# Kernel tuning notes

Measured on AMD Instinct MI355X. Metric: run time of the kernel, lower is better.

Reference implementation:

```python
import jax, jax.numpy as jnp
import numpy as np

# dims: batch, d_features(m), n_subsets, sub_size(k=ceil(m/n)), heads, d_k, d_v, conv kernel, d_out
B, M, N, K, H, DK, DV, KER, D = 512, 4096, 64, 64, 8, 32, 4, 3, 4096
DOUT_PER = D // N  # d_out_per_subset = 64
EPS_LN = 1e-5      # torch nn.LayerNorm default eps


def setup_inputs() -> dict:
    key = jax.random.key(0)
    ks = jax.random.split(key, 8)
    s = 0.02  # xavier-like scale
    return {
        "features": jax.random.normal(ks[0], (B, M), dtype=jnp.float32),
        # per-head permutation of the m feature indices (f_shuffle(m, h, seeds))
        "shuffled_index": jnp.argsort(jax.random.uniform(ks[1], (H, M)), axis=1).astype(jnp.int32),
        "gamma": jnp.ones((M,), jnp.float32),
        "beta": jnp.zeros((M,), jnp.float32),
        "W_q": (jax.random.normal(ks[2], (H * DK, K)) * s).astype(jnp.float32),   # Linear(k, h*d_k)
        "W_k": (jax.random.normal(ks[3], (H, DK, K)) * s).astype(jnp.float32),    # grouped Conv1d(h, h*d_k, kernel=k, stride=k)
        "W_v1": (jax.random.normal(ks[4], (H, DV, KER)) * s).astype(jnp.float32), # grouped Conv1d(h, h*d_v, kernel)
        "W_v2": (jax.random.normal(ks[5], (H, DV)) * s).astype(jnp.float32),      # grouped Conv1d(h*d_v, h, 1)
        "W_fc": (jax.random.normal(ks[6], (DOUT_PER, H * K)) * s).astype(jnp.float32),
    }


def reference(features, shuffled_index, gamma, beta, W_q, W_k, W_v1, W_v2, W_fc):
    b = features.shape[0]
    # LayerNorm over m (query path only)
    mu = features.mean(-1, keepdims=True)
    var = ((features - mu) ** 2).mean(-1, keepdims=True)
    q_in = (features - mu) / jnp.sqrt(var + EPS_LN) * gamma + beta

    # shuffled gather: [b, H, M]  (k*n == m here so k_pad/q_pad are no-ops)
    sf = features[:, shuffled_index]

    # query: [b, n, k] -> Linear(k, h*d_k) -> [b, H, N, DK]
    q = jnp.einsum('bnk,ek->bne', q_in.reshape(b, N, K), W_q)
    q = q.reshape(b, N, H, DK).transpose(0, 2, 1, 3)

    # key: grouped conv kernel=stride=k == per-subset contraction -> [b, H, DK, N]
    kf = sf.reshape(b, H, N, K)
    key_ = jnp.einsum('bhnk,hdk->bhdn', kf, W_k)

    # value: [b, N, H, K], right-pad by KER-1, depthwise conv -> relu -> 1x1 conv -> +residual
    v = kf.transpose(0, 2, 1, 3)  # [b, N, H, K]
    vp = jnp.pad(v, ((0, 0), (0, 0), (0, 0), (0, KER - 1)))
    win = jnp.stack([vp[..., t:t + K] for t in range(KER)], axis=-1)  # [b,N,H,K,KER]
    v1 = jnp.einsum('bnhpt,hdt->bnhdp', win, W_v1)
    v2 = jnp.einsum('bnhdp,hd->bnhp', jax.nn.relu(v1), W_v2)
    v = (v2 + v).transpose(0, 2, 1, 3)  # [b, H, N, K]

    # scaled dot-product attention, temperature = sqrt(m)
    attn = jax.nn.softmax(jnp.einsum('bhqd,bhdk->bhqk', q, key_) / jnp.sqrt(jnp.float32(M)), axis=-1)
    out = jnp.einsum('bhqk,bhks->bhqs', attn, v)           # [b, H, N, K]
    out = out.transpose(0, 2, 1, 3).reshape(b, N, H * K)   # [b, N, H*K]
    out = jnp.einsum('bnf,of->bno', out, W_fc).reshape(b, N * DOUT_PER)
    return out, attn.reshape(b * H, N, N)
```

## Files before the change

kernel.cpp:

```cpp
#include <hip/hip_runtime.h>

typedef __bf16 v8bf __attribute__((ext_vector_type(8)));
typedef __bf16 v4bf __attribute__((ext_vector_type(4)));
typedef __bf16 v2bf __attribute__((ext_vector_type(2)));
typedef float  v4f  __attribute__((ext_vector_type(4)));
typedef float  v2f  __attribute__((ext_vector_type(2)));
typedef unsigned long long u64;

namespace {

constexpr int kB = 512, kM = 4096, kH = 8;


__global__ __launch_bounds__(256) void k0_weights(
    const float* __restrict__ Wq, const float* __restrict__ Wk,
    const float* __restrict__ Wfc,
    __bf16* __restrict__ wq, __bf16* __restrict__ wk, __bf16* __restrict__ wfc,
    float* __restrict__ out) {
  int i = blockIdx.x * 256 + threadIdx.x;
  float4 z = make_float4(0.f, 0.f, 0.f, 0.f);
#pragma unroll
  for (int j = 0; j < 4; ++j) reinterpret_cast<float4*>(out)[i + j * 131072] = z;
  if (i < 16384) {
    int e = i >> 6, k = i & 63;
    int dst = ((e >> 4) * 2 + (k >> 5)) * 512 + (e & 15) * 32 + (k & 31);
    wq[dst] = (__bf16)(Wq[i] * 0.015625f);
  } else if (i < 32768) {
    int j = i - 16384;
    int e = j >> 6, k = j & 63;
    int dst = ((e >> 4) * 2 + (k >> 5)) * 512 + (e & 15) * 32 + (k & 31);
    wk[dst] = (__bf16)Wk[j];
  } else if (i < 65536) {
    int j = i - 32768;
    int o = j >> 9, f = j & 511;
    int dst = ((o >> 4) * 16 + (f >> 5)) * 512 + (o & 15) * 32 + (f & 31);
    wfc[dst] = (__bf16)Wfc[j];
  }
}

__global__ __launch_bounds__(256, 4) void k_fused(
    const float* __restrict__ feat, const int* __restrict__ sidx,
    const float* __restrict__ gamma, const float* __restrict__ beta,
    const __bf16* __restrict__ wq, const __bf16* __restrict__ wk,
    const float* __restrict__ Wv1, const float* __restrict__ Wv2,
    const __bf16* __restrict__ wfc, float* __restrict__ out) {
  __shared__ __align__(16) __bf16 smem[19968];
  __shared__ float red[4];
  __bf16* s_feat = smem;
  __bf16* s_qin  = smem + 4096;
  __bf16* s_kf   = smem + 8192;
  __bf16* s_K    = smem + 12800;
  __bf16* s_vT   = smem + 15360;
  __bf16* s_sc   = s_kf;

  const int b = blockIdx.x, half = blockIdx.y, h0 = 4 * half;
  const int t = threadIdx.x, w = t >> 6, lane = t & 63;
  const int quad = lane >> 4, l16 = lane & 15;
  const int myrow = 16 * w + l16;

  const float4* frow4 = reinterpret_cast<const float4*>(feat + (size_t)b * kM);
  const float4* g4  = reinterpret_cast<const float4*>(gamma);
  const float4* be4 = reinterpret_cast<const float4*>(beta);
  float4 xs[4];
  float s = 0.f;
#pragma unroll
  for (int j = 0; j < 4; ++j) {
    xs[j] = frow4[t + j * 256];
    s += xs[j].x + xs[j].y + xs[j].z + xs[j].w;
  }
  int4 idxc[4], idxn[4];
  {
    const int* ibase = sidx + (size_t)h0 * kM + myrow * 64 + 8 * quad;
#pragma unroll
    for (int p = 0; p < 4; ++p)
      idxc[p] = *(const int4*)(ibase + 32 * (p >> 1) + 4 * (p & 1));
  }
#pragma unroll
  for (int o = 32; o > 0; o >>= 1) s += __shfl_xor(s, o);
  if (lane == 0) red[w] = s;
  __syncthreads();
  const float mu = (red[0] + red[1] + red[2] + red[3]) * (1.f / kM);
  float var_p = 0.f;
#pragma unroll
  for (int j = 0; j < 4; ++j) {
    float d0 = xs[j].x - mu, d1 = xs[j].y - mu, d2 = xs[j].z - mu, d3 = xs[j].w - mu;
    var_p += d0 * d0 + d1 * d1 + d2 * d2 + d3 * d3;
  }
#pragma unroll
  for (int o = 32; o > 0; o >>= 1) var_p += __shfl_xor(var_p, o);
  __syncthreads();
  if (lane == 0) red[w] = var_p;
  __syncthreads();
  const float var  = (red[0] + red[1] + red[2] + red[3]) * (1.f / kM);
  const float rstd = rsqrtf(var + 1e-5f);
#pragma unroll
  for (int j = 0; j < 4; ++j) {
    const int i4 = t + j * 256;
    float4 g = g4[i4], bt = be4[i4];
    v4bf fb, qb;
    fb[0] = (__bf16)xs[j].x; fb[1] = (__bf16)xs[j].y;
    fb[2] = (__bf16)xs[j].z; fb[3] = (__bf16)xs[j].w;
    qb[0] = (__bf16)((xs[j].x - mu) * rstd * g.x + bt.x);
    qb[1] = (__bf16)((xs[j].y - mu) * rstd * g.y + bt.y);
    qb[2] = (__bf16)((xs[j].z - mu) * rstd * g.z + bt.z);
    qb[3] = (__bf16)((xs[j].w - mu) * rstd * g.w + bt.w);
    *(v4bf*)(s_feat + 4 * i4) = fb;
    const int n = i4 >> 4, k = 4 * (t & 15);
    const int dst = ((n >> 4) * 2 + (k >> 5)) * 512 + (n & 15) * 32 + (k & 31);
    *(v4bf*)(s_qin + dst) = qb;
  }
  __syncthreads();

  v4f acc[4] = {{0.f, 0.f, 0.f, 0.f}, {0.f, 0.f, 0.f, 0.f},
                {0.f, 0.f, 0.f, 0.f}, {0.f, 0.f, 0.f, 0.f}};

  for (int it = 0; it < 4; ++it) {
    const int h = h0 + it;

    v8bf aq;
    {
      v4f dq0 = {0.f, 0.f, 0.f, 0.f}, dq1 = {0.f, 0.f, 0.f, 0.f};
#pragma unroll
      for (int kt = 0; kt < 2; ++kt) {
        v8bf a  = *(const v8bf*)(s_qin + (2 * w + kt) * 512 + l16 * 32 + 8 * quad);
        v8bf b0 = *(const v8bf*)(wq + (size_t)(4 * h + kt) * 512 + l16 * 32 + 8 * quad);
        v8bf b1 = *(const v8bf*)(wq + (size_t)(4 * h + 2 + kt) * 512 + l16 * 32 + 8 * quad);
        dq0 = __builtin_amdgcn_mfma_f32_16x16x32_bf16(b0, a, dq0, 0, 0, 0);
        dq1 = __builtin_amdgcn_mfma_f32_16x16x32_bf16(b1, a, dq1, 0, 0, 0);
      }
      v4bf p0, p1;
#pragma unroll
      for (int r = 0; r < 4; ++r) { p0[r] = (__bf16)dq0[r]; p1[r] = (__bf16)dq1[r]; }
      const u64 P0 = __builtin_bit_cast(u64, p0), P1 = __builtin_bit_cast(u64, p1);
      const int qs = 16 * (2 * (quad & 1));
      u64 s0p0 = __shfl(P0, l16 + qs),      s0p1 = __shfl(P1, l16 + qs);
      u64 s1p0 = __shfl(P0, l16 + qs + 16), s1p1 = __shfl(P1, l16 + qs + 16);
      v4bf lo = __builtin_bit_cast(v4bf, (quad >> 1) ? s0p1 : s0p0);
      v4bf hi = __builtin_bit_cast(v4bf, (quad >> 1) ? s1p1 : s1p0);
#pragma unroll
      for (int r = 0; r < 4; ++r) { aq[r] = lo[r]; aq[4 + r] = hi[r]; }
    }

    if (it < 3) {
      const int* ibase = sidx + (size_t)(h + 1) * kM + myrow * 64 + 8 * quad;
#pragma unroll
      for (int p = 0; p < 4; ++p)
        idxn[p] = *(const int4*)(ibase + 32 * (p >> 1) + 4 * (p & 1));
    }

    v8bf a0, a1;
    a0[0] = s_feat[idxc[0].x]; a0[1] = s_feat[idxc[0].y];
    a0[2] = s_feat[idxc[0].z]; a0[3] = s_feat[idxc[0].w];
    a0[4] = s_feat[idxc[1].x]; a0[5] = s_feat[idxc[1].y];
    a0[6] = s_feat[idxc[1].z]; a0[7] = s_feat[idxc[1].w];
    a1[0] = s_feat[idxc[2].x]; a1[1] = s_feat[idxc[2].y];
    a1[2] = s_feat[idxc[2].z]; a1[3] = s_feat[idxc[2].w];
    a1[4] = s_feat[idxc[3].x]; a1[5] = s_feat[idxc[3].y];
    a1[6] = s_feat[idxc[3].z]; a1[7] = s_feat[idxc[3].w];
    *(v8bf*)(s_kf + myrow * 72 + 8 * quad)      = a0;
    *(v8bf*)(s_kf + myrow * 72 + 32 + 8 * quad) = a1;
    if (t < 64) { v8bf z = {}; *(v8bf*)(s_kf + t * 72 + 64) = z; }

    {
      v4f dk0 = {0.f, 0.f, 0.f, 0.f}, dk1 = {0.f, 0.f, 0.f, 0.f};
      v8bf b00 = *(const v8bf*)(wk + (size_t)(4 * h + 0) * 512 + l16 * 32 + 8 * quad);
      v8bf b10 = *(const v8bf*)(wk + (size_t)(4 * h + 2) * 512 + l16 * 32 + 8 * quad);
      dk0 = __builtin_amdgcn_mfma_f32_16x16x32_bf16(b00, a0, dk0, 0, 0, 0);
      dk1 = __builtin_amdgcn_mfma_f32_16x16x32_bf16(b10, a0, dk1, 0, 0, 0);
      v8bf b01 = *(const v8bf*)(wk + (size_t)(4 * h + 1) * 512 + l16 * 32 + 8 * quad);
      v8bf b11 = *(const v8bf*)(wk + (size_t)(4 * h + 3) * 512 + l16 * 32 + 8 * quad);
      dk0 = __builtin_amdgcn_mfma_f32_16x16x32_bf16(b01, a1, dk0, 0, 0, 0);
      dk1 = __builtin_amdgcn_mfma_f32_16x16x32_bf16(b11, a1, dk1, 0, 0, 0);
      v4bf p0, p1;
#pragma unroll
      for (int r = 0; r < 4; ++r) { p0[r] = (__bf16)dk0[r]; p1[r] = (__bf16)dk1[r]; }
      *(v4bf*)(s_K + myrow * 40 + 4 * quad)      = p0;
      *(v4bf*)(s_K + myrow * 40 + 16 + 4 * quad) = p1;
    }
    __syncthreads();

    {
      const int n = lane, p0c = w * 16;
      float w1[4][3], w2[4];
#pragma unroll
      for (int d = 0; d < 4; ++d) {
#pragma unroll
        for (int c = 0; c < 3; ++c) w1[d][c] = Wv1[(h * 4 + d) * 3 + c];
        w2[d] = Wv2[h * 4 + d];
      }
      v8bf xa = *(const v8bf*)(s_kf + n * 72 + p0c);
      v8bf xb = *(const v8bf*)(s_kf + n * 72 + p0c + 8);
      v2bf xc = *(const v2bf*)(s_kf + n * 72 + p0c + 16);
      v2f x2[10];
#pragma unroll
      for (int j = 0; j < 8; ++j) { x2[j][0] = (float)xa[j]; x2[j][1] = (float)xb[j]; }
      x2[8][0] = (float)xb[0]; x2[8][1] = (float)xc[0];
      x2[9][0] = (float)xb[1]; x2[9][1] = (float)xc[1];
      const v2f z2 = {0.f, 0.f};
#pragma unroll
      for (int pp = 0; pp < 8; ++pp) {
        v2f a2 = x2[pp];
#pragma unroll
        for (int d = 0; d < 4; ++d) {
          v2f v1 = x2[pp] * w1[d][0] + x2[pp + 1] * w1[d][1] + x2[pp + 2] * w1[d][2];
          v1 = __builtin_elementwise_max(v1, z2);
          a2 = a2 + v1 * w2[d];
        }
        s_vT[(p0c + pp) * 72 + n]     = (__bf16)a2[0];
        s_vT[(p0c + pp + 8) * 72 + n] = (__bf16)a2[1];
      }
    }
    __syncthreads();

    {
      v4f ds[4] = {{0.f, 0.f, 0.f, 0.f}, {0.f, 0.f, 0.f, 0.f},
                   {0.f, 0.f, 0.f, 0.f}, {0.f, 0.f, 0.f, 0.f}};
#pragma unroll
      for (int nt = 0; nt < 4; ++nt) {
        v8bf bb = *(const v8bf*)(s_K + (16 * nt + l16) * 40 + 8 * quad);
        ds[nt] = __builtin_amdgcn_mfma_f32_16x16x32_bf16(aq, bb, ds[nt], 0, 0, 0);
      }
#pragma unroll
      for (int nt = 0; nt < 4; ++nt)
#pragma unroll
        for (int r = 0; r < 4; ++r)
          s_sc[(16 * w + 4 * quad + r) * 72 + 16 * nt + l16] = (__bf16)ds[nt][r];
    }

    float* attn_out = out + (size_t)kB * kM + ((size_t)(b * kH + h)) * 4096;
#pragma unroll
    for (int rr = 0; rr < 4; ++rr) {
      const int row = 16 * w + 4 * rr + quad;
      v4bf pv = *(const v4bf*)(s_sc + row * 72 + 4 * l16);
      float e0 = (float)pv[0], e1 = (float)pv[1], e2 = (float)pv[2], e3 = (float)pv[3];
      float mx = fmaxf(fmaxf(e0, e1), fmaxf(e2, e3));
#pragma unroll
      for (int mk = 8; mk > 0; mk >>= 1) mx = fmaxf(mx, __shfl_xor(mx, mk));
      e0 = __expf(e0 - mx); e1 = __expf(e1 - mx);
      e2 = __expf(e2 - mx); e3 = __expf(e3 - mx);
      float ssum = e0 + e1 + e2 + e3;
#pragma unroll
      for (int mk = 8; mk > 0; mk >>= 1) ssum += __shfl_xor(ssum, mk);
      const float inv = 1.0f / ssum;
      e0 *= inv; e1 *= inv; e2 *= inv; e3 *= inv;
      *(float4*)(attn_out + row * 64 + 4 * l16) = make_float4(e0, e1, e2, e3);
      v4bf st;
      st[0] = (__bf16)e0; st[1] = (__bf16)e1; st[2] = (__bf16)e2; st[3] = (__bf16)e3;
      *(v4bf*)(s_sc + row * 72 + 4 * l16) = st;
    }

    v4f dO[4] = {{0.f, 0.f, 0.f, 0.f}, {0.f, 0.f, 0.f, 0.f},
                 {0.f, 0.f, 0.f, 0.f}, {0.f, 0.f, 0.f, 0.f}};
#pragma unroll
    for (int kt = 0; kt < 2; ++kt) {
      v8bf a = *(const v8bf*)(s_sc + (16 * w + l16) * 72 + 32 * kt + 8 * quad);
#pragma unroll
      for (int st = 0; st < 4; ++st) {
        v8bf bb = *(const v8bf*)(s_vT + (16 * st + l16) * 72 + 32 * kt + 8 * quad);
        dO[st] = __builtin_amdgcn_mfma_f32_16x16x32_bf16(a, bb, dO[st], 0, 0, 0);
      }
    }

    {
      __bf16* ob = s_kf + w * 1152;
#pragma unroll
      for (int st = 0; st < 4; ++st)
#pragma unroll
        for (int r = 0; r < 4; ++r)
          ob[(st >> 1) * 512 + (4 * quad + r) * 32 + (st & 1) * 16 + l16] = (__bf16)dO[st][r];
#pragma unroll
      for (int kt = 0; kt < 2; ++kt) {
        v8bf a = *(const v8bf*)(ob + kt * 512 + l16 * 32 + 8 * quad);
#pragma unroll
        for (int nt = 0; nt < 4; ++nt) {
          v8bf bb = *(const v8bf*)(wfc + (size_t)(nt * 16 + h * 2 + kt) * 512 + l16 * 32 + 8 * quad);
          acc[nt] = __builtin_amdgcn_mfma_f32_16x16x32_bf16(a, bb, acc[nt], 0, 0, 0);
        }
      }
    }
    __syncthreads();

    if (it < 3) {
#pragma unroll
      for (int p = 0; p < 4; ++p) idxc[p] = idxn[p];
    }
  }

  float* orow = out + (size_t)b * kM;
#pragma unroll
  for (int nt = 0; nt < 4; ++nt)
#pragma unroll
    for (int r = 0; r < 4; ++r)
      atomicAdd(&orow[(16 * w + 4 * quad + r) * 64 + 16 * nt + l16], acc[nt][r]);
}

}

extern "C" void kernel_launch(void* const* d_in, const int* in_sizes, int n_in,
                              void* d_out, int out_size, void* d_ws, size_t ws_size,
                              hipStream_t stream) {
  (void)in_sizes; (void)n_in; (void)out_size; (void)ws_size;
  const float* features = (const float*)d_in[0];
  const int*   sidx     = (const int*)d_in[1];
  const float* gamma    = (const float*)d_in[2];
  const float* beta     = (const float*)d_in[3];
  const float* Wq       = (const float*)d_in[4];
  const float* Wk       = (const float*)d_in[5];
  const float* Wv1      = (const float*)d_in[6];
  const float* Wv2      = (const float*)d_in[7];
  const float* Wfc      = (const float*)d_in[8];
  float* out = (float*)d_out;

  char* ws = (char*)d_ws;
  __bf16* ws_wq  = (__bf16*)(ws);
  __bf16* ws_wk  = (__bf16*)(ws + 32768);
  __bf16* ws_wfc = (__bf16*)(ws + 65536);

  hipLaunchKernelGGL(k0_weights, dim3(512), dim3(256), 0, stream,
                     Wq, Wk, Wfc, ws_wq, ws_wk, ws_wfc, out);
  hipLaunchKernelGGL(k_fused, dim3(kB, 2), dim3(256), 0, stream,
                     features, sidx, gamma, beta, ws_wq, ws_wk, Wv1, Wv2, ws_wfc, out);
}
```

Before: 136.2 us.

## Keep attention scores in registers and re-layout MFMA operands via lane shuffles

The score MFMA now uses swapped operands, so each lane holds a full transposed row slice and the softmax runs directly on registers with two cross-lane shuffles instead of a bf16 round-trip through shared memory. The probabilities and the P·V output are rearranged into MFMA A-operand layout with __shfl rather than being written to and re-read from LDS. This also keeps softmax inputs in fp32 instead of rounding the scores to bf16. The zero-padding store is hoisted out of the head loop and the trailing barrier moves earlier. The cost is extra shuffle and select instructions and higher register pressure, in exchange for removing LDS traffic and its bank conflicts.

```diff
diff --git a/kernel.cpp b/kernel.cpp
--- a/kernel.cpp
+++ b/kernel.cpp
@@ -51,7 +51,6 @@
   __bf16* s_kf   = smem + 8192;
   __bf16* s_K    = smem + 12800;
   __bf16* s_vT   = smem + 15360;
-  __bf16* s_sc   = s_kf;
 
   const int b = blockIdx.x, half = blockIdx.y, h0 = 4 * half;
   const int t = threadIdx.x, w = t >> 6, lane = t & 63;
@@ -109,6 +108,7 @@
     const int dst = ((n >> 4) * 2 + (k >> 5)) * 512 + (n & 15) * 32 + (k & 31);
     *(v4bf*)(s_qin + dst) = qb;
   }
+  if (t < 64) { v8bf z = {}; *(v8bf*)(s_kf + t * 72 + 64) = z; }
   __syncthreads();
 
   v4f acc[4] = {{0.f, 0.f, 0.f, 0.f}, {0.f, 0.f, 0.f, 0.f},
@@ -159,7 +159,6 @@
     a1[6] = s_feat[idxc[3].z]; a1[7] = s_feat[idxc[3].w];
     *(v8bf*)(s_kf + myrow * 72 + 8 * quad)      = a0;
     *(v8bf*)(s_kf + myrow * 72 + 32 + 8 * quad) = a1;
-    if (t < 64) { v8bf z = {}; *(v8bf*)(s_kf + t * 72 + 64) = z; }
 
     {
       v4f dk0 = {0.f, 0.f, 0.f, 0.f}, dk1 = {0.f, 0.f, 0.f, 0.f};
@@ -212,73 +211,92 @@
     }
     __syncthreads();
 
-    {
-      v4f ds[4] = {{0.f, 0.f, 0.f, 0.f}, {0.f, 0.f, 0.f, 0.f},
-                   {0.f, 0.f, 0.f, 0.f}, {0.f, 0.f, 0.f, 0.f}};
-#pragma unroll
-      for (int nt = 0; nt < 4; ++nt) {
-        v8bf bb = *(const v8bf*)(s_K + (16 * nt + l16) * 40 + 8 * quad);
-        ds[nt] = __builtin_amdgcn_mfma_f32_16x16x32_bf16(aq, bb, ds[nt], 0, 0, 0);
-      }
-#pragma unroll
-      for (int nt = 0; nt < 4; ++nt)
-#pragma unroll
-        for (int r = 0; r < 4; ++r)
-          s_sc[(16 * w + 4 * quad + r) * 72 + 16 * nt + l16] = (__bf16)ds[nt][r];
-    }
+    v4f sc[4];
+#pragma unroll
+    for (int nt = 0; nt < 4; ++nt) {
+      v4f zz = {0.f, 0.f, 0.f, 0.f};
+      v8bf bbK = *(const v8bf*)(s_K + (16 * nt + l16) * 40 + 8 * quad);
+      sc[nt] = __builtin_amdgcn_mfma_f32_16x16x32_bf16(bbK, aq, zz, 0, 0, 0);
+    }
+
+    float mx = sc[0][0];
+#pragma unroll
+    for (int nt = 0; nt < 4; ++nt)
+#pragma unroll
+      for (int r = 0; r < 4; ++r) mx = fmaxf(mx, sc[nt][r]);
+    mx = fmaxf(mx, __shfl_xor(mx, 16));
+    mx = fmaxf(mx, __shfl_xor(mx, 32));
+    float ssum = 0.f;
+#pragma unroll
+    for (int nt = 0; nt < 4; ++nt)
+#pragma unroll
+      for (int r = 0; r < 4; ++r) {
+        float e = __expf(sc[nt][r] - mx);
+        sc[nt][r] = e; ssum += e;
+      }
+    ssum += __shfl_xor(ssum, 16);
+    ssum += __shfl_xor(ssum, 32);
+    const float inv = 1.0f / ssum;
+#pragma unroll
+    for (int nt = 0; nt < 4; ++nt) sc[nt] *= inv;
 
     float* attn_out = out + (size_t)kB * kM + ((size_t)(b * kH + h)) * 4096;
 #pragma unroll
-    for (int rr = 0; rr < 4; ++rr) {
-      const int row = 16 * w + 4 * rr + quad;
-      v4bf pv = *(const v4bf*)(s_sc + row * 72 + 4 * l16);
-      float e0 = (float)pv[0], e1 = (float)pv[1], e2 = (float)pv[2], e3 = (float)pv[3];
-      float mx = fmaxf(fmaxf(e0, e1), fmaxf(e2, e3));
-#pragma unroll
-      for (int mk = 8; mk > 0; mk >>= 1) mx = fmaxf(mx, __shfl_xor(mx, mk));
-      e0 = __expf(e0 - mx); e1 = __expf(e1 - mx);
-      e2 = __expf(e2 - mx); e3 = __expf(e3 - mx);
-      float ssum = e0 + e1 + e2 + e3;
-#pragma unroll
-      for (int mk = 8; mk > 0; mk >>= 1) ssum += __shfl_xor(ssum, mk);
-      const float inv = 1.0f / ssum;
-      e0 *= inv; e1 *= inv; e2 *= inv; e3 *= inv;
-      *(float4*)(attn_out + row * 64 + 4 * l16) = make_float4(e0, e1, e2, e3);
-      v4bf st;
-      st[0] = (__bf16)e0; st[1] = (__bf16)e1; st[2] = (__bf16)e2; st[3] = (__bf16)e3;
-      *(v4bf*)(s_sc + row * 72 + 4 * l16) = st;
-    }
-
-    v4f dO[4] = {{0.f, 0.f, 0.f, 0.f}, {0.f, 0.f, 0.f, 0.f},
-                 {0.f, 0.f, 0.f, 0.f}, {0.f, 0.f, 0.f, 0.f}};
+    for (int nt = 0; nt < 4; ++nt)
+      *(v4f*)(attn_out + myrow * 64 + 16 * nt + 4 * quad) = sc[nt];
+
+    v4bf P[4];
+#pragma unroll
+    for (int nt = 0; nt < 4; ++nt)
+#pragma unroll
+      for (int r = 0; r < 4; ++r) P[nt][r] = (__bf16)sc[nt][r];
+
+    v4f dOT[4] = {{0.f, 0.f, 0.f, 0.f}, {0.f, 0.f, 0.f, 0.f},
+                  {0.f, 0.f, 0.f, 0.f}, {0.f, 0.f, 0.f, 0.f}};
+    const int src0 = l16 + 16 * (2 * (quad & 1));
 #pragma unroll
     for (int kt = 0; kt < 2; ++kt) {
-      v8bf a = *(const v8bf*)(s_sc + (16 * w + l16) * 72 + 32 * kt + 8 * quad);
+      const u64 pA = __builtin_bit_cast(u64, P[2 * kt]);
+      const u64 pB = __builtin_bit_cast(u64, P[2 * kt + 1]);
+      u64 A0 = __shfl(pA, src0), A1 = __shfl(pA, src0 + 16);
+      u64 B0 = __shfl(pB, src0), B1 = __shfl(pB, src0 + 16);
+      v4bf lo = __builtin_bit_cast(v4bf, (quad >> 1) ? B0 : A0);
+      v4bf hi = __builtin_bit_cast(v4bf, (quad >> 1) ? B1 : A1);
+      v8bf a_pv;
+#pragma unroll
+      for (int r = 0; r < 4; ++r) { a_pv[r] = lo[r]; a_pv[4 + r] = hi[r]; }
 #pragma unroll
       for (int st = 0; st < 4; ++st) {
         v8bf bb = *(const v8bf*)(s_vT + (16 * st + l16) * 72 + 32 * kt + 8 * quad);
-        dO[st] = __builtin_amdgcn_mfma_f32_16x16x32_bf16(a, bb, dO[st], 0, 0, 0);
-      }
-    }
+        dOT[st] = __builtin_amdgcn_mfma_f32_16x16x32_bf16(bb, a_pv, dOT[st], 0, 0, 0);
+      }
+    }
+    __syncthreads();
 
     {
-      __bf16* ob = s_kf + w * 1152;
+      v4bf Q[4];
 #pragma unroll
       for (int st = 0; st < 4; ++st)
 #pragma unroll
-        for (int r = 0; r < 4; ++r)
-          ob[(st >> 1) * 512 + (4 * quad + r) * 32 + (st & 1) * 16 + l16] = (__bf16)dO[st][r];
+        for (int r = 0; r < 4; ++r) Q[st][r] = (__bf16)dOT[st][r];
 #pragma unroll
       for (int kt = 0; kt < 2; ++kt) {
-        v8bf a = *(const v8bf*)(ob + kt * 512 + l16 * 32 + 8 * quad);
+        const u64 qA = __builtin_bit_cast(u64, Q[2 * kt]);
+        const u64 qB = __builtin_bit_cast(u64, Q[2 * kt + 1]);
+        u64 A0 = __shfl(qA, src0), A1 = __shfl(qA, src0 + 16);
+        u64 B0 = __shfl(qB, src0), B1 = __shfl(qB, src0 + 16);
+        v4bf lo = __builtin_bit_cast(v4bf, (quad >> 1) ? B0 : A0);
+        v4bf hi = __builtin_bit_cast(v4bf, (quad >> 1) ? B1 : A1);
+        v8bf a_fc;
+#pragma unroll
+        for (int r = 0; r < 4; ++r) { a_fc[r] = lo[r]; a_fc[4 + r] = hi[r]; }
 #pragma unroll
         for (int nt = 0; nt < 4; ++nt) {
           v8bf bb = *(const v8bf*)(wfc + (size_t)(nt * 16 + h * 2 + kt) * 512 + l16 * 32 + 8 * quad);
-          acc[nt] = __builtin_amdgcn_mfma_f32_16x16x32_bf16(a, bb, acc[nt], 0, 0, 0);
+          acc[nt] = __builtin_amdgcn_mfma_f32_16x16x32_bf16(a_fc, bb, acc[nt], 0, 0, 0);
         }
       }
     }
-    __syncthreads();
 
     if (it < 3) {
 #pragma unroll
```

After: 135.9 us. About the same (-0.2%).
